# Optimization experiments

Hardware: AMD Instinct MI355X
Metric: run time of the kernel (lower is better)

## Reference

```python
import jax, jax.numpy as jnp
import numpy as np

K = 3
TOP_K = 10
MASK_RATIO = 0.5
EPS_COS = 1e-8
EPS_DEG = 1e-6


def setup_inputs() -> dict:
    key = jax.random.key(0)
    ks = jax.random.split(key, 10)
    N, C, H, O, E = 4096, 128, 128, 64, 65536
    x = jax.random.normal(ks[0], (N, C), dtype=jnp.float32)
    edge_index = jax.random.randint(ks[1], (2, E), 0, N, dtype=jnp.int64)
    alpha = jnp.full((K,), 1.0 / K, dtype=jnp.float32)
    fusion_W = 0.02 * jax.random.normal(ks[2], (2 * H, H), dtype=jnp.float32)
    fusion_b = jnp.zeros((H,), dtype=jnp.float32)
    lin0_W = 0.02 * jax.random.normal(ks[3], (C, H), dtype=jnp.float32)
    lin0_b = jnp.zeros((H,), dtype=jnp.float32)
    lin1_W = 0.02 * jax.random.normal(ks[4], (H, O), dtype=jnp.float32)
    lin1_b = jnp.zeros((O,), dtype=jnp.float32)
    return {
        "x": x, "edge_index": edge_index, "alpha": alpha,
        "fusion_W": fusion_W, "fusion_b": fusion_b,
        "lin0_W": lin0_W, "lin0_b": lin0_b,
        "lin1_W": lin1_W, "lin1_b": lin1_b,
    }


def reference(x, edge_index, alpha, fusion_W, fusion_b, lin0_W, lin0_b, lin1_W, lin1_b):
    N = x.shape[0]
    # dense adjacency and its powers: A^0 = I (so A^0 @ x = x), A^1, A^2
    A = jnp.zeros((N, N), x.dtype).at[edge_index[0], edge_index[1]].set(1.0)
    A2 = A @ A
    hop_feats = jnp.stack([x, A @ x, A2 @ x], axis=0)  # [K, N, C]

    # per-node cosine-similarity top-k (self always included, cos=1)
    xn = x / (jnp.linalg.norm(x, axis=-1, keepdims=True) + EPS_COS)
    sim = xn @ xn.T  # [N, N]
    _, topk_idx = jax.lax.top_k(sim, TOP_K)  # [N, TOP_K]

    # random keep-mask per node, forced True at top-k neighbors
    mask = jax.random.uniform(jax.random.key(42), (N, N)) < MASK_RATIO
    rows = jnp.arange(N)[:, None]
    mask = mask.at[rows, topk_idx].set(True)
    Mf = mask.astype(x.dtype)  # [N, N]

    # alpha-weighted multi-hop aggregate, masked mean over selected nodes
    agg = jnp.einsum('k,knc->nc', alpha, hop_feats)  # [N, C]
    fused = (Mf @ agg) / (Mf.sum(axis=1, keepdims=True) + EPS_DEG)  # [N, C]

    h = jnp.concatenate([x, fused], axis=-1) @ fusion_W + fusion_b
    h = jax.nn.relu(h @ lin0_W + lin0_b)  # dropout inactive in eval
    out = h @ lin1_W + lin1_b
    return jax.nn.log_softmax(out, axis=1)
```

## Files before the change

### kernel.cpp

```cpp
#include <hip/hip_runtime.h>
#include <hip/hip_bf16.h>
#include <stdint.h>


#define N_NODES 4096
#define C_DIM   128
#define WPR     128
#define HALF_P  8388608u
#define TOPK    10
#define LSTR    13
#define JSPLIT  4
#define KSPLIT  2

typedef __attribute__((ext_vector_type(8))) short bf16x8;
typedef __attribute__((ext_vector_type(4))) float f32x4;

__device__ __forceinline__ uint16_t f2bf(float f) {
    uint32_t u = __float_as_uint(f);
    return (uint16_t)((u + 0x7FFFu + ((u >> 16) & 1u)) >> 16);
}

__device__ __forceinline__ uint32_t rotl32(uint32_t v, int r) {
    return (v << r) | (v >> (32 - r));
}

__device__ __forceinline__ void threefry2x32(uint32_t k0, uint32_t k1,
                                             uint32_t x0, uint32_t x1,
                                             uint32_t& o0, uint32_t& o1) {
    uint32_t ks2 = k0 ^ k1 ^ 0x1BD11BDAu;
    x0 += k0; x1 += k1;
#define TF_ROUND(r) { x0 += x1; x1 = rotl32(x1, (r)); x1 ^= x0; }
    TF_ROUND(13) TF_ROUND(15) TF_ROUND(26) TF_ROUND(6)
    x0 += k1;  x1 += ks2 + 1u;
    TF_ROUND(17) TF_ROUND(29) TF_ROUND(16) TF_ROUND(24)
    x0 += ks2; x1 += k0 + 2u;
    TF_ROUND(13) TF_ROUND(15) TF_ROUND(26) TF_ROUND(6)
    x0 += k0;  x1 += k1 + 3u;
    TF_ROUND(17) TF_ROUND(29) TF_ROUND(16) TF_ROUND(24)
    x0 += k1;  x1 += ks2 + 4u;
    TF_ROUND(13) TF_ROUND(15) TF_ROUND(26) TF_ROUND(6)
    x0 += ks2; x1 += k0 + 5u;
#undef TF_ROUND
    o0 = x0; o1 = x1;
}

__global__ void scatter_kernel(const int* __restrict__ ei, int E,
                               uint32_t* __restrict__ Abits) {
    __shared__ int cnt_oddnz;
    int t = threadIdx.x;
    if (t == 0) cnt_oddnz = 0;
    __syncthreads();
    if (((const uint32_t*)ei)[2 * t + 1] != 0u) atomicAdd(&cnt_oddnz, 1);
    __syncthreads();
    bool is64 = (cnt_oddnz <= 8);
    int e = blockIdx.x * blockDim.x + t;
    if (e >= E) return;
    int src, dst;
    if (is64) { src = ei[2 * e]; dst = ei[2 * (E + e)]; }
    else      { src = ei[e];     dst = ei[E + e]; }
    src &= (N_NODES - 1);
    dst &= (N_NODES - 1);
    atomicOr(&Abits[src * WPR + (dst >> 5)], 1u << (dst & 31));
}

__global__ void spmm_kernel(const uint32_t* __restrict__ Abits,
                            const float* __restrict__ in,
                            float* __restrict__ out) {
    int i = blockIdx.x;
    int c = threadIdx.x;
    __shared__ uint32_t wbits[WPR];
    wbits[c] = Abits[i * WPR + c];
    __syncthreads();
    float acc = 0.f;
    for (int w = 0; w < WPR; ++w) {
        uint32_t bits = wbits[w];
        while (bits) {
            int b = __ffs(bits) - 1;
            bits &= bits - 1;
            acc += in[(w * 32 + b) * C_DIM + c];
        }
    }
    out[i * C_DIM + c] = acc;
}

__global__ void spmm2_combo_kernel(const uint32_t* __restrict__ Abits,
                                   const float* __restrict__ hop1,
                                   const float* __restrict__ xf,
                                   const float* __restrict__ alpha,
                                   float* __restrict__ agg,
                                   uint16_t* __restrict__ aggTb,
                                   uint16_t* __restrict__ xnb,
                                   uint32_t* __restrict__ Mbits,
                                   int* __restrict__ degInt) {
    int i = blockIdx.x;
    int c = threadIdx.x;
    __shared__ uint32_t wbits[WPR];
    __shared__ float ws[2];
    wbits[c] = Abits[i * WPR + c];
    __syncthreads();
    float acc = 0.f;
    for (int w = 0; w < WPR; ++w) {
        uint32_t bits = wbits[w];
        while (bits) {
            int b = __ffs(bits) - 1;
            bits &= bits - 1;
            acc += hop1[(w * 32 + b) * C_DIM + c];
        }
    }
    float xv  = xf[i * C_DIM + c];
    float h1v = hop1[i * C_DIM + c];
    float a = alpha[0] * xv + alpha[1] * h1v + alpha[2] * acc;
    agg[i * C_DIM + c] = a;
    aggTb[(size_t)c * N_NODES + i] = f2bf(a);

    float sq = xv * xv;
    #pragma unroll
    for (int off = 32; off >= 1; off >>= 1) sq += __shfl_xor(sq, off);
    if ((c & 63) == 0) ws[c >> 6] = sq;
    __syncthreads();
    float tot = ws[0] + ws[1];
    xnb[i * C_DIM + c] = f2bf(xv / (sqrtf(tot) + 1e-8f));

    uint32_t u = (uint32_t)(i * 128 + c);
    uint32_t tid = u >> 1;
    uint32_t halfb = u & 1u;
    uint32_t base = tid * 32u + halfb * 16u;
    uint32_t w0 = 0u, w1 = 0u;
    for (int k = 0; k < 16; ++k) {
        uint32_t o0, o1;
        threefry2x32(0u, 42u, base + k, HALF_P + base + k, o0, o1);
        w0 |= (uint32_t)((o0 >> 31) ^ 1u) << k;
        w1 |= (uint32_t)((o1 >> 31) ^ 1u) << k;
    }
    uint32_t w0o = (uint32_t)__shfl_xor((int)w0, 1);
    uint32_t w1o = (uint32_t)__shfl_xor((int)w1, 1);
    int p0 = 0, p1 = 0;
    if (halfb == 0u) {
        uint32_t W0 = w0 | (w0o << 16);
        uint32_t W1 = w1 | (w1o << 16);
        Mbits[tid] = W0;
        Mbits[(HALF_P >> 5) + tid] = W1;
        p0 = __popc(W0); p1 = __popc(W1);
    }
    #pragma unroll
    for (int off = 32; off >= 1; off >>= 1) {
        p0 += __shfl_xor(p0, off);
        p1 += __shfl_xor(p1, off);
    }
    if ((c & 63) == 0) {
        int row0 = i >> 1;
        atomicAdd(&degInt[row0], p0);
        atomicAdd(&degInt[2048 + row0], p1);
    }
}

__launch_bounds__(512, 4)
__global__ void topk_kernel(const uint16_t* __restrict__ xnb,
                            float* __restrict__ topv,
                            int* __restrict__ topi) {
    int i0 = blockIdx.x * 16;
    int part = blockIdx.y;
    int t = threadIdx.x;
    int w = t >> 6;
    int lane = t & 63;
    int col = lane & 15;
    int quad = lane >> 4;

    __shared__ float    sval[32 * 16 * LSTR];
    __shared__ uint16_t sidx[32 * 16 * LSTR];

    bf16x8 bfi[4];
    #pragma unroll
    for (int s = 0; s < 4; ++s)
        bfi[s] = *(const bf16x8*)&xnb[(size_t)(i0 + col) * C_DIM + s * 32 + quad * 8];

    float tv[TOPK]; int ti[TOPK];
    #pragma unroll
    for (int k = 0; k < TOPK; ++k) { tv[k] = -1e30f; ti[k] = 0xFFFF; }

    int jt0 = part * 64 + w * 8;
    for (int p = 0; p < 8; ++p) {
        int j0 = (jt0 + p) * 16;
        f32x4 acc = {0.f, 0.f, 0.f, 0.f};
        #pragma unroll
        for (int s = 0; s < 4; ++s) {
            bf16x8 aj = *(const bf16x8*)&xnb[(size_t)(j0 + col) * C_DIM + s * 32 + quad * 8];
            acc = __builtin_amdgcn_mfma_f32_16x16x32_bf16(aj, bfi[s], acc, 0, 0, 0);
        }
        float m4 = fmaxf(fmaxf(acc[0], acc[1]), fmaxf(acc[2], acc[3]));
        if (m4 > tv[TOPK-1]) {
            #pragma unroll
            for (int r = 0; r < 4; ++r) {
                float d = acc[r];
                if (d > tv[TOPK-1]) {
                    int j = j0 + quad * 4 + r;
                    tv[TOPK-1] = d; ti[TOPK-1] = j;
                    #pragma unroll
                    for (int q = TOPK - 2; q >= 0; --q) {
                        if (tv[q+1] > tv[q]) {
                            float fv = tv[q]; tv[q] = tv[q+1]; tv[q+1] = fv;
                            int iv = ti[q];  ti[q] = ti[q+1];  ti[q+1] = iv;
                        }
                    }
                }
            }
        }
    }

    int base = ((w * 4 + quad) * 16 + col) * LSTR;
    #pragma unroll
    for (int k = 0; k < TOPK; ++k) {
        sval[base + k] = tv[k];
        sidx[base + k] = (uint16_t)ti[k];
    }

    int row = t & 15, L = t >> 4;
    for (int s = 16; s >= 1; s >>= 1) {
        __syncthreads();
        if (L < s) {
            int la = (L * 16 + row) * LSTR;
            int lb = ((L + s) * 16 + row) * LSTR;
            float ov[TOPK]; uint16_t oi[TOPK];
            int ia = 0, ib = 0;
            #pragma unroll
            for (int k = 0; k < TOPK; ++k) {
                float va = sval[la + ia], vb = sval[lb + ib];
                uint16_t xa = sidx[la + ia], xb = sidx[lb + ib];
                bool takeA = (va > vb) || (va == vb && xa < xb);
                if (takeA) { ov[k] = va; oi[k] = xa; ++ia; }
                else       { ov[k] = vb; oi[k] = xb; ++ib; }
            }
            #pragma unroll
            for (int k = 0; k < TOPK; ++k) { sval[la + k] = ov[k]; sidx[la + k] = oi[k]; }
        }
    }
    __syncthreads();
    if (t < 16) {
        size_t gi = (size_t)(part * N_NODES + i0 + t) * TOPK;
        #pragma unroll
        for (int k = 0; k < TOPK; ++k) {
            topv[gi + k] = sval[t * LSTR + k];
            topi[gi + k] = (int)sidx[t * LSTR + k];
        }
    }
}

__launch_bounds__(512, 4)
__global__ void fused_kernel(const uint32_t* __restrict__ Mbits,
                             const uint16_t* __restrict__ aggTb,
                             const float* __restrict__ topv,
                             const int* __restrict__ topi,
                             int* __restrict__ degInt,
                             float* __restrict__ fpart) {
    int i0 = blockIdx.x * 16;
    int part = blockIdx.y;
    int t = threadIdx.x;
    int w = t >> 6;
    int lane = t & 63;
    int col = lane & 15;
    int quad = lane >> 4;

    __shared__ uint32_t smask[16][65];
    __shared__ float    lv[16][JSPLIT][TOPK];
    __shared__ uint16_t li[16][JSPLIT][TOPK];
    for (int r = t; r < 16 * 64; r += 512)
        smask[r >> 6][r & 63] =
            Mbits[(size_t)(i0 + (r >> 6)) * WPR + part * 64 + (r & 63)];
    if (t < 16 * JSPLIT) {
        int row = t & 15, q = t >> 4;
        size_t gi = (size_t)(q * N_NODES + i0 + row) * TOPK;
        #pragma unroll
        for (int k = 0; k < TOPK; ++k) {
            lv[row][q][k] = topv[gi + k];
            li[row][q][k] = (uint16_t)topi[gi + k];
        }
    }
    __syncthreads();

    if (t < 16) {
        int ix[JSPLIT] = {0, 0, 0, 0};
        int newc = 0;
        int kw0 = part * 2048;
        #pragma unroll
        for (int k = 0; k < TOPK; ++k) {
            float bestv = -1e38f; int bestj = 0x7fffffff; int bestq = 0;
            #pragma unroll
            for (int q = 0; q < JSPLIT; ++q) {
                bool ok = ix[q] < TOPK;
                float fv = ok ? lv[t][q][ix[q]] : -1e38f;
                int   jj = ok ? (int)li[t][q][ix[q]] : 0x7fffffff;
                if (fv > bestv || (fv == bestv && jj < bestj)) {
                    bestv = fv; bestj = jj; bestq = q;
                }
            }
            ++ix[bestq];
            int rel = bestj - kw0;
            if (rel >= 0 && rel < 2048) {
                uint32_t* wp = &smask[t][rel >> 5];
                uint32_t old = *wp, bit = 1u << (bestj & 31);
                newc += (int)((old & bit) == 0u);
                *wp = old | bit;
            }
        }
        if (newc) atomicAdd(&degInt[i0 + t], newc);
    }
    __syncthreads();

    const uint16_t* brow = aggTb + (size_t)(w * 16 + col) * N_NODES;
    int kbase = part * 2048;
    f32x4 acc[4];
    #pragma unroll
    for (int u = 0; u < 4; ++u) acc[u] = (f32x4){0.f, 0.f, 0.f, 0.f};

    for (int k0 = 0; k0 < 2048; k0 += 128) {
        #pragma unroll
        for (int u = 0; u < 4; ++u) {
            uint32_t mw = smask[col][(k0 >> 5) + u];
            uint32_t byte = (mw >> (quad * 8)) & 0xFFu;
            union { uint32_t uu[4]; bf16x8 v; } a;
            #pragma unroll
            for (int pp = 0; pp < 4; ++pp) {
                uint32_t lo = (byte >> (2 * pp)) & 1u;
                uint32_t hi = (byte >> (2 * pp + 1)) & 1u;
                a.uu[pp] = (lo ? 0x3F80u : 0u) | (hi ? 0x3F800000u : 0u);
            }
            bf16x8 b = *(const bf16x8*)&brow[kbase + k0 + u * 32 + quad * 8];
            acc[u] = __builtin_amdgcn_mfma_f32_16x16x32_bf16(a.v, b, acc[u], 0, 0, 0);
        }
    }
    #pragma unroll
    for (int r = 0; r < 4; ++r) {
        int il = quad * 4 + r;
        float s = (acc[0][r] + acc[1][r]) + (acc[2][r] + acc[3][r]);
        fpart[(size_t)part * (N_NODES * C_DIM)
              + (size_t)(i0 + il) * C_DIM + w * 16 + col] = s;
    }
}

__global__ void mlp_kernel(const float* __restrict__ xf,
                           const float* __restrict__ fpart,
                           const int* __restrict__ degInt,
                           const float* __restrict__ fW, const float* __restrict__ fB,
                           const float* __restrict__ l0W, const float* __restrict__ l0B,
                           const float* __restrict__ l1W, const float* __restrict__ l1B,
                           float* __restrict__ out) {
    int i0 = blockIdx.x * 4;
    int t = threadIdx.x;
    __shared__ float lx[4][256];
    __shared__ float hb[4][128];
    const float* f0 = fpart;
    const float* f1 = fpart + (size_t)N_NODES * C_DIM;
    for (int r = t; r < 4 * 128; r += 128) {
        int row = r >> 7, c = r & 127;
        size_t idx = (size_t)(i0 + row) * C_DIM + c;
        lx[row][c] = xf[idx];
        lx[row][128 + c] = (f0[idx] + f1[idx])
                           / ((float)degInt[i0 + row] + 1e-6f);
    }
    __syncthreads();
    float acc[4];
    #pragma unroll
    for (int r = 0; r < 4; ++r) acc[r] = fB[t];
    for (int k = 0; k < 256; ++k) {
        float wv = fW[k * 128 + t];
        #pragma unroll
        for (int r = 0; r < 4; ++r) acc[r] = fmaf(lx[r][k], wv, acc[r]);
    }
    #pragma unroll
    for (int r = 0; r < 4; ++r) hb[r][t] = acc[r];
    __syncthreads();
    #pragma unroll
    for (int r = 0; r < 4; ++r) acc[r] = l0B[t];
    for (int k = 0; k < 128; ++k) {
        float wv = l0W[k * 128 + t];
        #pragma unroll
        for (int r = 0; r < 4; ++r) acc[r] = fmaf(hb[r][k], wv, acc[r]);
    }
    __syncthreads();
    #pragma unroll
    for (int r = 0; r < 4; ++r) lx[r][t] = fmaxf(acc[r], 0.f);
    __syncthreads();
    int o = t & 63, pr = t >> 6;
    #pragma unroll
    for (int rr = 0; rr < 2; ++rr) {
        int r = pr + 2 * rr;
        float a = l1B[o];
        for (int k = 0; k < 128; ++k)
            a = fmaf(lx[r][k], l1W[k * 64 + o], a);
        float m = a;
        #pragma unroll
        for (int off = 32; off >= 1; off >>= 1) m = fmaxf(m, __shfl_xor(m, off));
        float e = expf(a - m);
        float s = e;
        #pragma unroll
        for (int off = 32; off >= 1; off >>= 1) s += __shfl_xor(s, off);
        out[(size_t)(i0 + r) * 64 + o] = a - m - logf(s);
    }
}

extern "C" void kernel_launch(void* const* d_in, const int* in_sizes, int n_in,
                              void* d_out, int out_size, void* d_ws, size_t ws_size,
                              hipStream_t stream) {
    const float* xf    = (const float*)d_in[0];
    const int*   ei    = (const int*)d_in[1];
    const float* alpha = (const float*)d_in[2];
    const float* fW    = (const float*)d_in[3];
    const float* fB    = (const float*)d_in[4];
    const float* l0W   = (const float*)d_in[5];
    const float* l0B   = (const float*)d_in[6];
    const float* l1W   = (const float*)d_in[7];
    const float* l1B   = (const float*)d_in[8];
    float* out = (float*)d_out;
    const int E  = in_sizes[1] / 2;
    const int NC = N_NODES * C_DIM;

    char* p = (char*)d_ws;
    const size_t SZ = (size_t)NC * 4;
    uint32_t* Abits  = (uint32_t*)p; p += SZ;
    int*      degInt = (int*)p;      p += N_NODES * 4;
    float*    hop1   = (float*)p;    p += SZ;
    float*    agg    = (float*)p;    p += SZ;
    uint32_t* Mbits  = (uint32_t*)p; p += SZ;
    float*    fpart  = (float*)p;    p += KSPLIT * SZ;
    uint16_t* xnb    = (uint16_t*)p; p += SZ / 2;
    uint16_t* aggTb  = (uint16_t*)p; p += SZ / 2;
    float*    topv   = (float*)p;    p += (size_t)JSPLIT * N_NODES * TOPK * 4;
    int*      topi   = (int*)p;      p += (size_t)JSPLIT * N_NODES * TOPK * 4;

    hipMemsetAsync(Abits, 0, SZ + N_NODES * 4, stream);
    scatter_kernel<<<(E + 255) / 256, 256, 0, stream>>>(ei, E, Abits);
    spmm_kernel<<<N_NODES, 128, 0, stream>>>(Abits, xf, hop1);
    spmm2_combo_kernel<<<N_NODES, 128, 0, stream>>>(Abits, hop1, xf, alpha,
                                                    agg, aggTb, xnb, Mbits, degInt);
    topk_kernel<<<dim3(N_NODES / 16, JSPLIT), 512, 0, stream>>>(xnb, topv, topi);
    fused_kernel<<<dim3(N_NODES / 16, KSPLIT), 512, 0, stream>>>(Mbits, aggTb,
                                                                 topv, topi,
                                                                 degInt, fpart);
    mlp_kernel<<<N_NODES / 4, 128, 0, stream>>>(xf, fpart, degInt,
                                                fW, fB, l0W, l0B, l1W, l1B, out);
}
```

Measured before the change: 229.2 us.

## Move x normalization into first SpMM and co-schedule second hop with top-k

The bf16 normalized-x computation moves into the first SpMM kernel, so top-k no longer depends on the second-hop kernel. The second-hop SpMM, aggregation and random-mask generation are then merged with the cosine top-k into one launch of 2048 blocks: the first 1024 blocks do top-k and the rest do the hop-2 work, four rows per block. This removes a launch and lets the ALU-heavy threefry mask generation overlap with the MFMA-heavy similarity search. In exchange, both roles share one block size and one shared-memory allocation, and the 512-thread launch bounds may limit occupancy for the hop-2 part.

```diff
diff --git a/kernel.cpp b/kernel.cpp
--- a/kernel.cpp
+++ b/kernel.cpp
@@ -63,12 +63,14 @@
     atomicOr(&Abits[src * WPR + (dst >> 5)], 1u << (dst & 31));
 }
 
-__global__ void spmm_kernel(const uint32_t* __restrict__ Abits,
-                            const float* __restrict__ in,
-                            float* __restrict__ out) {
+__global__ void spmm_norm_kernel(const uint32_t* __restrict__ Abits,
+                                 const float* __restrict__ xf,
+                                 float* __restrict__ hop1,
+                                 uint16_t* __restrict__ xnb) {
     int i = blockIdx.x;
     int c = threadIdx.x;
     __shared__ uint32_t wbits[WPR];
+    __shared__ float ws[2];
     wbits[c] = Abits[i * WPR + c];
     __syncthreads();
     float acc = 0.f;
@@ -77,170 +79,173 @@
         while (bits) {
             int b = __ffs(bits) - 1;
             bits &= bits - 1;
-            acc += in[(w * 32 + b) * C_DIM + c];
-        }
-    }
-    out[i * C_DIM + c] = acc;
-}
-
-__global__ void spmm2_combo_kernel(const uint32_t* __restrict__ Abits,
-                                   const float* __restrict__ hop1,
-                                   const float* __restrict__ xf,
-                                   const float* __restrict__ alpha,
-                                   float* __restrict__ agg,
-                                   uint16_t* __restrict__ aggTb,
-                                   uint16_t* __restrict__ xnb,
-                                   uint32_t* __restrict__ Mbits,
-                                   int* __restrict__ degInt) {
-    int i = blockIdx.x;
-    int c = threadIdx.x;
-    __shared__ uint32_t wbits[WPR];
-    __shared__ float ws[2];
-    wbits[c] = Abits[i * WPR + c];
-    __syncthreads();
-    float acc = 0.f;
-    for (int w = 0; w < WPR; ++w) {
-        uint32_t bits = wbits[w];
-        while (bits) {
-            int b = __ffs(bits) - 1;
-            bits &= bits - 1;
-            acc += hop1[(w * 32 + b) * C_DIM + c];
-        }
-    }
-    float xv  = xf[i * C_DIM + c];
-    float h1v = hop1[i * C_DIM + c];
-    float a = alpha[0] * xv + alpha[1] * h1v + alpha[2] * acc;
-    agg[i * C_DIM + c] = a;
-    aggTb[(size_t)c * N_NODES + i] = f2bf(a);
-
-    float sq = xv * xv;
+            acc += xf[(w * 32 + b) * C_DIM + c];
+        }
+    }
+    hop1[i * C_DIM + c] = acc;
+    float v = xf[i * C_DIM + c];
+    float sq = v * v;
     #pragma unroll
     for (int off = 32; off >= 1; off >>= 1) sq += __shfl_xor(sq, off);
     if ((c & 63) == 0) ws[c >> 6] = sq;
     __syncthreads();
     float tot = ws[0] + ws[1];
-    xnb[i * C_DIM + c] = f2bf(xv / (sqrtf(tot) + 1e-8f));
-
-    uint32_t u = (uint32_t)(i * 128 + c);
-    uint32_t tid = u >> 1;
-    uint32_t halfb = u & 1u;
-    uint32_t base = tid * 32u + halfb * 16u;
-    uint32_t w0 = 0u, w1 = 0u;
-    for (int k = 0; k < 16; ++k) {
-        uint32_t o0, o1;
-        threefry2x32(0u, 42u, base + k, HALF_P + base + k, o0, o1);
-        w0 |= (uint32_t)((o0 >> 31) ^ 1u) << k;
-        w1 |= (uint32_t)((o1 >> 31) ^ 1u) << k;
-    }
-    uint32_t w0o = (uint32_t)__shfl_xor((int)w0, 1);
-    uint32_t w1o = (uint32_t)__shfl_xor((int)w1, 1);
-    int p0 = 0, p1 = 0;
-    if (halfb == 0u) {
-        uint32_t W0 = w0 | (w0o << 16);
-        uint32_t W1 = w1 | (w1o << 16);
-        Mbits[tid] = W0;
-        Mbits[(HALF_P >> 5) + tid] = W1;
-        p0 = __popc(W0); p1 = __popc(W1);
-    }
-    #pragma unroll
-    for (int off = 32; off >= 1; off >>= 1) {
-        p0 += __shfl_xor(p0, off);
-        p1 += __shfl_xor(p1, off);
-    }
-    if ((c & 63) == 0) {
-        int row0 = i >> 1;
-        atomicAdd(&degInt[row0], p0);
-        atomicAdd(&degInt[2048 + row0], p1);
-    }
+    xnb[i * C_DIM + c] = f2bf(v / (sqrtf(tot) + 1e-8f));
 }
 
 __launch_bounds__(512, 4)
-__global__ void topk_kernel(const uint16_t* __restrict__ xnb,
-                            float* __restrict__ topv,
-                            int* __restrict__ topi) {
-    int i0 = blockIdx.x * 16;
-    int part = blockIdx.y;
+__global__ void combo_topk_kernel(const uint32_t* __restrict__ Abits,
+                                  const float* __restrict__ hop1,
+                                  const float* __restrict__ xf,
+                                  const float* __restrict__ alpha,
+                                  float* __restrict__ agg,
+                                  uint16_t* __restrict__ aggTb,
+                                  const uint16_t* __restrict__ xnb,
+                                  uint32_t* __restrict__ Mbits,
+                                  int* __restrict__ degInt,
+                                  float* __restrict__ topv,
+                                  int* __restrict__ topi) {
+    __shared__ uint8_t smem[32 * 16 * LSTR * 6];
     int t = threadIdx.x;
-    int w = t >> 6;
-    int lane = t & 63;
-    int col = lane & 15;
-    int quad = lane >> 4;
-
-    __shared__ float    sval[32 * 16 * LSTR];
-    __shared__ uint16_t sidx[32 * 16 * LSTR];
-
-    bf16x8 bfi[4];
-    #pragma unroll
-    for (int s = 0; s < 4; ++s)
-        bfi[s] = *(const bf16x8*)&xnb[(size_t)(i0 + col) * C_DIM + s * 32 + quad * 8];
-
-    float tv[TOPK]; int ti[TOPK];
-    #pragma unroll
-    for (int k = 0; k < TOPK; ++k) { tv[k] = -1e30f; ti[k] = 0xFFFF; }
-
-    int jt0 = part * 64 + w * 8;
-    for (int p = 0; p < 8; ++p) {
-        int j0 = (jt0 + p) * 16;
-        f32x4 acc = {0.f, 0.f, 0.f, 0.f};
-        #pragma unroll
-        for (int s = 0; s < 4; ++s) {
-            bf16x8 aj = *(const bf16x8*)&xnb[(size_t)(j0 + col) * C_DIM + s * 32 + quad * 8];
-            acc = __builtin_amdgcn_mfma_f32_16x16x32_bf16(aj, bfi[s], acc, 0, 0, 0);
-        }
-        float m4 = fmaxf(fmaxf(acc[0], acc[1]), fmaxf(acc[2], acc[3]));
-        if (m4 > tv[TOPK-1]) {
+
+    if (blockIdx.x < 1024) {
+        float*    sval = (float*)smem;
+        uint16_t* sidx = (uint16_t*)(smem + 32 * 16 * LSTR * 4);
+        int it   = blockIdx.x & 255;
+        int part = blockIdx.x >> 8;
+        int i0 = it * 16;
+        int w = t >> 6;
+        int lane = t & 63;
+        int col = lane & 15;
+        int quad = lane >> 4;
+
+        bf16x8 bfi[4];
+        #pragma unroll
+        for (int s = 0; s < 4; ++s)
+            bfi[s] = *(const bf16x8*)&xnb[(size_t)(i0 + col) * C_DIM + s * 32 + quad * 8];
+
+        float tv[TOPK]; int ti[TOPK];
+        #pragma unroll
+        for (int k = 0; k < TOPK; ++k) { tv[k] = -1e30f; ti[k] = 0xFFFF; }
+
+        int jt0 = part * 64 + w * 8;
+        for (int p = 0; p < 8; ++p) {
+            int j0 = (jt0 + p) * 16;
+            f32x4 acc = {0.f, 0.f, 0.f, 0.f};
             #pragma unroll
-            for (int r = 0; r < 4; ++r) {
-                float d = acc[r];
-                if (d > tv[TOPK-1]) {
-                    int j = j0 + quad * 4 + r;
-                    tv[TOPK-1] = d; ti[TOPK-1] = j;
-                    #pragma unroll
-                    for (int q = TOPK - 2; q >= 0; --q) {
-                        if (tv[q+1] > tv[q]) {
-                            float fv = tv[q]; tv[q] = tv[q+1]; tv[q+1] = fv;
-                            int iv = ti[q];  ti[q] = ti[q+1];  ti[q+1] = iv;
+            for (int s = 0; s < 4; ++s) {
+                bf16x8 aj = *(const bf16x8*)&xnb[(size_t)(j0 + col) * C_DIM + s * 32 + quad * 8];
+                acc = __builtin_amdgcn_mfma_f32_16x16x32_bf16(aj, bfi[s], acc, 0, 0, 0);
+            }
+            float m4 = fmaxf(fmaxf(acc[0], acc[1]), fmaxf(acc[2], acc[3]));
+            if (m4 > tv[TOPK-1]) {
+                #pragma unroll
+                for (int r = 0; r < 4; ++r) {
+                    float d = acc[r];
+                    if (d > tv[TOPK-1]) {
+                        int j = j0 + quad * 4 + r;
+                        tv[TOPK-1] = d; ti[TOPK-1] = j;
+                        #pragma unroll
+                        for (int q = TOPK - 2; q >= 0; --q) {
+                            if (tv[q+1] > tv[q]) {
+                                float fv = tv[q]; tv[q] = tv[q+1]; tv[q+1] = fv;
+                                int iv = ti[q];  ti[q] = ti[q+1];  ti[q+1] = iv;
+                            }
                         }
                     }
                 }
             }
         }
-    }
-
-    int base = ((w * 4 + quad) * 16 + col) * LSTR;
-    #pragma unroll
-    for (int k = 0; k < TOPK; ++k) {
-        sval[base + k] = tv[k];
-        sidx[base + k] = (uint16_t)ti[k];
-    }
-
-    int row = t & 15, L = t >> 4;
-    for (int s = 16; s >= 1; s >>= 1) {
+
+        int base = ((w * 4 + quad) * 16 + col) * LSTR;
+        #pragma unroll
+        for (int k = 0; k < TOPK; ++k) {
+            sval[base + k] = tv[k];
+            sidx[base + k] = (uint16_t)ti[k];
+        }
+
+        int row = t & 15, L = t >> 4;
+        for (int s = 16; s >= 1; s >>= 1) {
+            __syncthreads();
+            if (L < s) {
+                int la = (L * 16 + row) * LSTR;
+                int lb = ((L + s) * 16 + row) * LSTR;
+                float ov[TOPK]; uint16_t oi[TOPK];
+                int ia = 0, ib = 0;
+                #pragma unroll
+                for (int k = 0; k < TOPK; ++k) {
+                    float va = sval[la + ia], vb = sval[lb + ib];
+                    uint16_t xa = sidx[la + ia], xb = sidx[lb + ib];
+                    bool takeA = (va > vb) || (va == vb && xa < xb);
+                    if (takeA) { ov[k] = va; oi[k] = xa; ++ia; }
+                    else       { ov[k] = vb; oi[k] = xb; ++ib; }
+                }
+                #pragma unroll
+                for (int k = 0; k < TOPK; ++k) { sval[la + k] = ov[k]; sidx[la + k] = oi[k]; }
+            }
+        }
         __syncthreads();
-        if (L < s) {
-            int la = (L * 16 + row) * LSTR;
-            int lb = ((L + s) * 16 + row) * LSTR;
-            float ov[TOPK]; uint16_t oi[TOPK];
-            int ia = 0, ib = 0;
+        if (t < 16) {
+            size_t gi = (size_t)(part * N_NODES + i0 + t) * TOPK;
             #pragma unroll
             for (int k = 0; k < TOPK; ++k) {
-                float va = sval[la + ia], vb = sval[lb + ib];
-                uint16_t xa = sidx[la + ia], xb = sidx[lb + ib];
-                bool takeA = (va > vb) || (va == vb && xa < xb);
-                if (takeA) { ov[k] = va; oi[k] = xa; ++ia; }
-                else       { ov[k] = vb; oi[k] = xb; ++ib; }
-            }
-            #pragma unroll
-            for (int k = 0; k < TOPK; ++k) { sval[la + k] = ov[k]; sidx[la + k] = oi[k]; }
-        }
-    }
-    __syncthreads();
-    if (t < 16) {
-        size_t gi = (size_t)(part * N_NODES + i0 + t) * TOPK;
-        #pragma unroll
-        for (int k = 0; k < TOPK; ++k) {
-            topv[gi + k] = sval[t * LSTR + k];
-            topi[gi + k] = (int)sidx[t * LSTR + k];
+                topv[gi + k] = sval[t * LSTR + k];
+                topi[gi + k] = (int)sidx[t * LSTR + k];
+            }
+        }
+    } else {
+        uint32_t* wb = (uint32_t*)smem;
+        int bid = blockIdx.x - 1024;
+        int sg = t >> 7;
+        int c  = t & 127;
+        int i  = bid * 4 + sg;
+        wb[sg * 128 + c] = Abits[i * WPR + c];
+        __syncthreads();
+        float acc = 0.f;
+        for (int w = 0; w < WPR; ++w) {
+            uint32_t bits = wb[sg * 128 + w];
+            while (bits) {
+                int b = __ffs(bits) - 1;
+                bits &= bits - 1;
+                acc += hop1[(w * 32 + b) * C_DIM + c];
+            }
+        }
+        float xv  = xf[i * C_DIM + c];
+        float h1v = hop1[i * C_DIM + c];
+        float a = alpha[0] * xv + alpha[1] * h1v + alpha[2] * acc;
+        agg[i * C_DIM + c] = a;
+        aggTb[(size_t)c * N_NODES + i] = f2bf(a);
+
+        uint32_t u = (uint32_t)(i * 128 + c);
+        uint32_t tid = u >> 1;
+        uint32_t halfb = u & 1u;
+        uint32_t base = tid * 32u + halfb * 16u;
+        uint32_t w0 = 0u, w1 = 0u;
+        for (int k = 0; k < 16; ++k) {
+            uint32_t o0, o1;
+            threefry2x32(0u, 42u, base + k, HALF_P + base + k, o0, o1);
+            w0 |= (uint32_t)((o0 >> 31) ^ 1u) << k;
+            w1 |= (uint32_t)((o1 >> 31) ^ 1u) << k;
+        }
+        uint32_t w0o = (uint32_t)__shfl_xor((int)w0, 1);
+        uint32_t w1o = (uint32_t)__shfl_xor((int)w1, 1);
+        int p0 = 0, p1 = 0;
+        if (halfb == 0u) {
+            uint32_t W0 = w0 | (w0o << 16);
+            uint32_t W1 = w1 | (w1o << 16);
+            Mbits[tid] = W0;
+            Mbits[(HALF_P >> 5) + tid] = W1;
+            p0 = __popc(W0); p1 = __popc(W1);
+        }
+        #pragma unroll
+        for (int off = 32; off >= 1; off >>= 1) {
+            p0 += __shfl_xor(p0, off);
+            p1 += __shfl_xor(p1, off);
+        }
+        if ((t & 63) == 0) {
+            int row0 = i >> 1;
+            atomicAdd(&degInt[row0], p0);
+            atomicAdd(&degInt[2048 + row0], p1);
         }
     }
 }
@@ -429,10 +434,10 @@
 
     hipMemsetAsync(Abits, 0, SZ + N_NODES * 4, stream);
     scatter_kernel<<<(E + 255) / 256, 256, 0, stream>>>(ei, E, Abits);
-    spmm_kernel<<<N_NODES, 128, 0, stream>>>(Abits, xf, hop1);
-    spmm2_combo_kernel<<<N_NODES, 128, 0, stream>>>(Abits, hop1, xf, alpha,
-                                                    agg, aggTb, xnb, Mbits, degInt);
-    topk_kernel<<<dim3(N_NODES / 16, JSPLIT), 512, 0, stream>>>(xnb, topv, topi);
+    spmm_norm_kernel<<<N_NODES, 128, 0, stream>>>(Abits, xf, hop1, xnb);
+    combo_topk_kernel<<<2048, 512, 0, stream>>>(Abits, hop1, xf, alpha,
+                                                agg, aggTb, xnb, Mbits, degInt,
+                                                topv, topi);
     fused_kernel<<<dim3(N_NODES / 16, KSPLIT), 512, 0, stream>>>(Mbits, aggTb,
                                                                  topv, topi,
                                                                  degInt, fpart);
```

Measured after the change: 226.9 us. Within noise of the previous version (-1.0%).
